# Performance work log

Measured on AMD Instinct MI355X. Metric: run time of the kernel, lower is better.

Reference implementation:

```python
import jax, jax.numpy as jnp
import numpy as np

TOP_K = 2


def setup_inputs() -> dict:
    key = jax.random.key(0)
    ks = jax.random.split(key, 5)
    B, S, D, F, E = 2, 2048, 1024, 3584, 8
    scale_in = 1.0 / np.sqrt(D)
    scale_f = 1.0 / np.sqrt(F)
    return {
        "hidden_states": jax.random.normal(ks[0], (B, S, D), dtype=jnp.float32),
        "gate_w": jax.random.normal(ks[1], (E, D), dtype=jnp.float32) * scale_in,
        "w1": jax.random.normal(ks[2], (E, F, D), dtype=jnp.float32) * scale_in,
        "w3": jax.random.normal(ks[3], (E, F, D), dtype=jnp.float32) * scale_in,
        "w2": jax.random.normal(ks[4], (E, D, F), dtype=jnp.float32) * scale_f,
    }


def _routing_weights(logits):
    # softmax over experts, select top-k, renormalize (Mixtral semantics)
    probs = jax.nn.softmax(logits, axis=-1)          # [T, E]
    topv, topi = jax.lax.top_k(probs, TOP_K)          # [T, k]
    topv = topv / jnp.sum(topv, axis=-1, keepdims=True)
    T, E = logits.shape
    w = jnp.zeros((T, E), dtype=logits.dtype)
    w = w.at[jnp.arange(T)[:, None], topi].set(topv)  # dense [T, E] routing weights
    return w


def reference(hidden_states, gate_w, w1, w3, w2):
    B, S, D = hidden_states.shape
    x = hidden_states.reshape(-1, D)                  # [T, D]
    logits = x @ gate_w.T                             # [T, E]
    rw = _routing_weights(logits)                     # [T, E]
    E = gate_w.shape[0]
    out = jnp.zeros_like(x)
    for e in range(E):                                # fixed small expert count
        h = jax.nn.silu(x @ w1[e].T) * (x @ w3[e].T)  # [T, F]
        out = out + rw[:, e:e + 1] * (h @ w2[e].T)    # [T, D]
    return out.reshape(B, S, D)
```

## Files before the change

### kernel.cpp

```cpp
#include <hip/hip_runtime.h>
#include <hip/hip_bf16.h>


#define T_TOK 4096
#define DIM   1024
#define FF    3584
#define NE    8
#define CAP   (T_TOK*2 + NE*256)

#define OFF_TOPI   256UL
#define OFF_TOPW   33024UL
#define OFF_ROWTOK 65792UL
#define OFF_TOKPOS 106752UL
#define OFF_W1B    147712UL
#define OFF_W3B    (OFF_W1B + 58720256UL)
#define OFF_W2B    OFF_W1B
#define OFF_RES    OFF_W3B
#define OFF_H      (OFF_W1B + 117440512UL)
#define WS_NEED    (OFF_H + 73400320UL)

using f32x4 = __attribute__((ext_vector_type(4))) float;
using s16x8 = __attribute__((ext_vector_type(8))) short;

__device__ __forceinline__ ushort f2b(float f) {
    __hip_bfloat16 b = __float2bfloat16(f);
    ushort u; __builtin_memcpy(&u, &b, 2); return u;
}
__device__ __forceinline__ float blo(uint u){ u <<= 16; float f; __builtin_memcpy(&f,&u,4); return f; }
__device__ __forceinline__ float bhi(uint u){ u &= 0xFFFF0000u; float f; __builtin_memcpy(&f,&u,4); return f; }
__device__ __forceinline__ void gl_lds16(const ushort* g, ushort* l) {
    __builtin_amdgcn_global_load_lds(
        (const __attribute__((address_space(1))) void*)g,
        (__attribute__((address_space(3))) void*)l, 16, 0, 0);
}
__device__ __forceinline__ uint4 pack8(float4 v0, float4 v1) {
    uint4 o;
    o.x = f2b(v0.x) | ((uint)f2b(v0.y) << 16);
    o.y = f2b(v0.z) | ((uint)f2b(v0.w) << 16);
    o.z = f2b(v1.x) | ((uint)f2b(v1.y) << 16);
    o.w = f2b(v1.z) | ((uint)f2b(v1.w) << 16);
    return o;
}

#define VMC(n) asm volatile("s_waitcnt vmcnt(" #n ")" ::: "memory")
#define BAR()  __builtin_amdgcn_s_barrier()

__global__ __launch_bounds__(256)
void k_route(const float* __restrict__ x, const float* __restrict__ gw,
             int* __restrict__ topi, float* __restrict__ topw,
             int* __restrict__ counts, ushort* __restrict__ xb)
{
    __shared__ float gws[NE*DIM];
    const int tid = threadIdx.x;
    for (int i = tid; i < NE*DIM/4; i += 256)
        ((float4*)gws)[i] = ((const float4*)gw)[i];
    __syncthreads();

    const int lane = tid & 63, wid = tid >> 6;
    const int t = blockIdx.x*4 + wid;

    float4 xr[4];
    const float4* xrow = (const float4*)(x + (size_t)t*DIM) + lane*4;
    #pragma unroll
    for (int i = 0; i < 4; ++i) xr[i] = xrow[i];

    uint4* xbd = (uint4*)(xb + (size_t)t*DIM);
    xbd[lane*2]   = pack8(xr[0], xr[1]);
    xbd[lane*2+1] = pack8(xr[2], xr[3]);

    float lg[NE];
    #pragma unroll
    for (int e = 0; e < NE; ++e) {
        const float4* g4 = (const float4*)(gws + e*DIM) + lane*4;
        float s = 0.f;
        #pragma unroll
        for (int i = 0; i < 4; ++i) {
            float4 g = g4[i];
            s += xr[i].x*g.x + xr[i].y*g.y + xr[i].z*g.z + xr[i].w*g.w;
        }
        #pragma unroll
        for (int off = 32; off; off >>= 1) s += __shfl_xor(s, off);
        lg[e] = s;
    }
    if (lane == 0) {
        float b1 = -1e30f, b2 = -1e30f; int i1 = 0, i2 = 0;
        #pragma unroll
        for (int e = 0; e < NE; ++e) {
            float v = lg[e];
            if (v > b1)      { b2 = b1; i2 = i1; b1 = v; i1 = e; }
            else if (v > b2) { b2 = v; i2 = e; }
        }
        float p2 = __expf(b2 - b1);
        float inv = 1.f / (1.f + p2);
        topi[2*t]   = i1; topi[2*t+1] = i2;
        topw[2*t]   = inv; topw[2*t+1] = p2*inv;
        atomicAdd(&counts[i1], 1); atomicAdd(&counts[i2], 1);
    }
}

__global__ void k_scan(const int* __restrict__ counts, int* __restrict__ offs,
                       int* __restrict__ rowTok)
{
    if (threadIdx.x == 0) {
        int acc = 0; offs[0] = 0;
        for (int e = 0; e < NE; ++e) {
            int p = (counts[e] + 255) & ~255;
            acc += p; offs[e+1] = acc;
        }
    }
    for (int i = threadIdx.x; i < CAP; i += blockDim.x) rowTok[i] = -1;
}

__global__ __launch_bounds__(256)
void k_scatter(const int* __restrict__ topi,
               const int* __restrict__ offs, int* __restrict__ cursor,
               int* __restrict__ rowTok, int* __restrict__ tokPos)
{
    int t = blockIdx.x*256 + threadIdx.x;
    #pragma unroll
    for (int j = 0; j < 2; ++j) {
        int e = topi[2*t + j];
        int pos = offs[e] + atomicAdd(&cursor[e], 1);
        rowTok[pos] = t;
        tokPos[2*t + j] = pos;
    }
}

__global__ __launch_bounds__(256)
void k_cvt(const float* __restrict__ src, ushort* __restrict__ dst)
{
    size_t i = (size_t)blockIdx.x*256 + threadIdx.x;
    float4 v0 = ((const float4*)src)[2*i], v1 = ((const float4*)src)[2*i+1];
    ((uint4*)dst)[i] = pack8(v0, v1);
}

#define CVT_HALF ((NE*FF*DIM/8)/256)
__global__ __launch_bounds__(256)
void k_cvt2(const float* __restrict__ w1, const float* __restrict__ w3,
            ushort* __restrict__ w1b, ushort* __restrict__ w3b)
{
    int b = blockIdx.x;
    const float* src; ushort* dst;
    if (b < CVT_HALF) { src = w1; dst = w1b; }
    else              { src = w3; dst = w3b; b -= CVT_HALF; }
    size_t i = (size_t)b*256 + threadIdx.x;
    float4 v0 = ((const float4*)src)[2*i], v1 = ((const float4*)src)[2*i+1];
    ((uint4*)dst)[i] = pack8(v0, v1);
}

#define G1_SLOT 12288
__global__ __launch_bounds__(256, 2)
void k_gemm1(const ushort* __restrict__ xb,
             const ushort* __restrict__ w1b, const ushort* __restrict__ w3b,
             const int* __restrict__ offs, const int* __restrict__ rowTok,
             ushort* __restrict__ hout)
{
    __shared__ __align__(16) ushort L[3*G1_SLOT];
    const int sb = blockIdx.x;
    const int rowStart = blockIdx.y * 256;
    if (rowStart >= offs[8]) return;
    int e = 0;
    #pragma unroll
    for (int k = 1; k < NE; ++k) if (rowStart >= offs[k]) e = k;

    const int tid = threadIdx.x, lane = tid & 63, wid = tid >> 6;
    const int wr = wid >> 1, wc = wid & 1;
    const int lo = lane & 15, hi = lane >> 4;

    const int srow = lane >> 2;
    const int sch  = (lane & 3) ^ ((lane >> 3) & 3);
    const ushort* aS[4];
    #pragma unroll
    for (int j = 0; j < 4; ++j) {
        int tk = rowTok[rowStart + j*64 + wid*16 + srow]; if (tk < 0) tk = 0;
        aS[j] = xb + (size_t)tk*DIM + sch*8;
    }
    const ushort* bS[2];
    bS[0] = w1b + ((size_t)e*FF + sb*64 + wid*16 + srow)*DIM + sch*8;
    bS[1] = w3b + ((size_t)e*FF + sb*64 + wid*16 + srow)*DIM + sch*8;
    ushort* const dA = L + wid*512;
    ushort* const dB = L + 8192 + wid*512;

    const int sig = (lo >> 1) & 3;
    const int roff = ((hi ^ sig) * 8);
    int rdA[8], rdB[4];
    #pragma unroll
    for (int m = 0; m < 8; ++m) rdA[m] = (wr*128 + m*16 + lo)*32 + roff;
    #pragma unroll
    for (int n = 0; n < 2; ++n) {
        rdB[n]   = 8192 + (wc*32 + n*16 + lo)*32 + roff;
        rdB[n+2] = 8192 + (64 + wc*32 + n*16 + lo)*32 + roff;
    }

    f32x4 acc[8][4];
    #pragma unroll
    for (int m = 0; m < 8; ++m)
        #pragma unroll
        for (int n = 0; n < 4; ++n) acc[m][n] = (f32x4)(0.f);

    #pragma unroll
    for (int t0 = 0; t0 < 2; ++t0) {
        #pragma unroll
        for (int j = 0; j < 4; ++j) gl_lds16(aS[j] + t0*32, dA + t0*G1_SLOT + j*2048);
        #pragma unroll
        for (int j = 0; j < 2; ++j) gl_lds16(bS[j] + t0*32, dB + t0*G1_SLOT + j*2048);
    }
    VMC(6);
    BAR();

    const int NK = DIM/32;
    int cur = 0, nxt = 2;
    for (int t = 0; t < NK; ++t) {
        const ushort* Lb = L + cur*G1_SLOT;
        const bool pf = (t + 2 < NK);
        s16x8 a[8], b[4];
        #pragma unroll
        for (int n = 0; n < 4; ++n) b[n] = *(const s16x8*)(Lb + rdB[n]);
        #pragma unroll
        for (int m = 0; m < 8; ++m) a[m] = *(const s16x8*)(Lb + rdA[m]);
        if (pf) {
            #pragma unroll
            for (int j = 0; j < 4; ++j)
                gl_lds16(aS[j] + (t+2)*32, dA + nxt*G1_SLOT + j*2048);
            gl_lds16(bS[0] + (t+2)*32, dB + nxt*G1_SLOT);
            gl_lds16(bS[1] + (t+2)*32, dB + nxt*G1_SLOT + 2048);
        }
        BAR();
        __builtin_amdgcn_s_setprio(1);
        #pragma unroll
        for (int m = 0; m < 8; ++m)
            #pragma unroll
            for (int n = 0; n < 4; ++n)
                acc[m][n] = __builtin_amdgcn_mfma_f32_16x16x32_bf16(a[m], b[n], acc[m][n], 0, 0, 0);
        __builtin_amdgcn_s_setprio(0);
        if (t < NK-2) { VMC(6); } else { VMC(0); }
        BAR();
        cur = (cur == 2) ? 0 : cur + 1;
        nxt = (nxt == 2) ? 0 : nxt + 1;
    }

    #pragma unroll
    for (int m = 0; m < 8; ++m)
        #pragma unroll
        for (int p = 0; p < 2; ++p) {
            f32x4 v1 = acc[m][p], v3 = acc[m][p+2];
            int f = sb*64 + wc*32 + p*16 + lo;
            #pragma unroll
            for (int j = 0; j < 4; ++j) {
                int row = rowStart + wr*128 + m*16 + hi*4 + j;
                float s = v1[j];
                float val = (s / (1.f + __expf(-s))) * v3[j];
                hout[(size_t)row*FF + f] = f2b(val);
            }
        }
}

__global__ __launch_bounds__(256, 2)
void k_gemm2(const ushort* __restrict__ h, const ushort* __restrict__ w2b,
             const int* __restrict__ offs, ushort* __restrict__ res)
{
    __shared__ __align__(16) ushort L[3*G1_SLOT];
    const int dc = blockIdx.x * 128;
    const int rowStart = blockIdx.y * 256;
    if (rowStart >= offs[8]) return;
    int e = 0;
    #pragma unroll
    for (int k = 1; k < NE; ++k) if (rowStart >= offs[k]) e = k;
    const int kbase = blockIdx.z * (FF/2);

    const int tid = threadIdx.x, lane = tid & 63, wid = tid >> 6;
    const int wr = wid >> 1, wc = wid & 1;
    const int lo = lane & 15, hi = lane >> 4;

    const int srow = lane >> 2;
    const int sch  = (lane & 3) ^ ((lane >> 3) & 3);
    const ushort* aS[4];
    #pragma unroll
    for (int j = 0; j < 4; ++j)
        aS[j] = h + (size_t)(rowStart + j*64 + wid*16 + srow)*FF + kbase + sch*8;
    const ushort* bS[2];
    #pragma unroll
    for (int j = 0; j < 2; ++j)
        bS[j] = w2b + ((size_t)e*DIM + dc + j*64 + wid*16 + srow)*FF + kbase + sch*8;
    ushort* const dA = L + wid*512;
    ushort* const dB = L + 8192 + wid*512;

    const int sig = (lo >> 1) & 3;
    const int roff = ((hi ^ sig) * 8);
    int rdA[8], rdB[4];
    #pragma unroll
    for (int m = 0; m < 8; ++m) rdA[m] = (wr*128 + m*16 + lo)*32 + roff;
    #pragma unroll
    for (int n = 0; n < 4; ++n) rdB[n] = 8192 + (wc*64 + n*16 + lo)*32 + roff;

    f32x4 acc[8][4];
    #pragma unroll
    for (int m = 0; m < 8; ++m)
        #pragma unroll
        for (int n = 0; n < 4; ++n) acc[m][n] = (f32x4)(0.f);

    #pragma unroll
    for (int t0 = 0; t0 < 2; ++t0) {
        #pragma unroll
        for (int j = 0; j < 4; ++j) gl_lds16(aS[j] + t0*32, dA + t0*G1_SLOT + j*2048);
        #pragma unroll
        for (int j = 0; j < 2; ++j) gl_lds16(bS[j] + t0*32, dB + t0*G1_SLOT + j*2048);
    }
    VMC(6);
    BAR();

    const int NK = (FF/2)/32;
    int cur = 0, nxt = 2;
    for (int t = 0; t < NK; ++t) {
        const ushort* Lb = L + cur*G1_SLOT;
        const bool pf = (t + 2 < NK);
        s16x8 a[8], b[4];
        #pragma unroll
        for (int n = 0; n < 4; ++n) b[n] = *(const s16x8*)(Lb + rdB[n]);
        #pragma unroll
        for (int m = 0; m < 8; ++m) a[m] = *(const s16x8*)(Lb + rdA[m]);
        if (pf) {
            #pragma unroll
            for (int j = 0; j < 4; ++j)
                gl_lds16(aS[j] + (t+2)*32, dA + nxt*G1_SLOT + j*2048);
            gl_lds16(bS[0] + (t+2)*32, dB + nxt*G1_SLOT);
            gl_lds16(bS[1] + (t+2)*32, dB + nxt*G1_SLOT + 2048);
        }
        BAR();
        __builtin_amdgcn_s_setprio(1);
        #pragma unroll
        for (int m = 0; m < 8; ++m)
            #pragma unroll
            for (int n = 0; n < 4; ++n)
                acc[m][n] = __builtin_amdgcn_mfma_f32_16x16x32_bf16(a[m], b[n], acc[m][n], 0, 0, 0);
        __builtin_amdgcn_s_setprio(0);
        if (t < NK-2) { VMC(6); } else { VMC(0); }
        BAR();
        cur = (cur == 2) ? 0 : cur + 1;
        nxt = (nxt == 2) ? 0 : nxt + 1;
    }

    ushort* rz = res + (size_t)blockIdx.z * CAP * DIM;
    #pragma unroll
    for (int m = 0; m < 8; ++m)
        #pragma unroll
        for (int j = 0; j < 4; ++j) {
            int prow = rowStart + wr*128 + m*16 + hi*4 + j;
            #pragma unroll
            for (int n = 0; n < 4; ++n) {
                int d = dc + wc*64 + n*16 + lo;
                rz[(size_t)prow*DIM + d] = f2b(acc[m][n][j]);
            }
        }
}

__global__ __launch_bounds__(256)
void k_combine(const ushort* __restrict__ res, const int* __restrict__ tokPos,
               const float* __restrict__ topw, float* __restrict__ out)
{
    int i = blockIdx.x*256 + threadIdx.x;
    int t = i >> 7;
    int g = i & 127;
    int pA = tokPos[2*t], pB = tokPos[2*t+1];
    float wA = topw[2*t], wB = topw[2*t+1];
    const ushort* res1 = res + (size_t)CAP * DIM;
    uint4 a0 = *(const uint4*)(res  + (size_t)pA*DIM + g*8);
    uint4 a1 = *(const uint4*)(res1 + (size_t)pA*DIM + g*8);
    uint4 b0 = *(const uint4*)(res  + (size_t)pB*DIM + g*8);
    uint4 b1 = *(const uint4*)(res1 + (size_t)pB*DIM + g*8);
    float4 o0, o1;
    o0.x = wA*(blo(a0.x)+blo(a1.x)) + wB*(blo(b0.x)+blo(b1.x));
    o0.y = wA*(bhi(a0.x)+bhi(a1.x)) + wB*(bhi(b0.x)+bhi(b1.x));
    o0.z = wA*(blo(a0.y)+blo(a1.y)) + wB*(blo(b0.y)+blo(b1.y));
    o0.w = wA*(bhi(a0.y)+bhi(a1.y)) + wB*(bhi(b0.y)+bhi(b1.y));
    o1.x = wA*(blo(a0.z)+blo(a1.z)) + wB*(blo(b0.z)+blo(b1.z));
    o1.y = wA*(bhi(a0.z)+bhi(a1.z)) + wB*(bhi(b0.z)+bhi(b1.z));
    o1.z = wA*(blo(a0.w)+blo(a1.w)) + wB*(blo(b0.w)+blo(b1.w));
    o1.w = wA*(bhi(a0.w)+bhi(a1.w)) + wB*(bhi(b0.w)+bhi(b1.w));
    float4* dst = (float4*)(out + (size_t)t*DIM + g*8);
    dst[0] = o0; dst[1] = o1;
}

extern "C" void kernel_launch(void* const* d_in, const int* in_sizes, int n_in,
                              void* d_out, int out_size, void* d_ws, size_t ws_size,
                              hipStream_t stream)
{
    const float* x  = (const float*)d_in[0];
    const float* gw = (const float*)d_in[1];
    const float* w1 = (const float*)d_in[2];
    const float* w3 = (const float*)d_in[3];
    const float* w2 = (const float*)d_in[4];
    float* out = (float*)d_out;
    char* ws = (char*)d_ws;
    if (ws_size < WS_NEED) return;

    int*    counts = (int*)ws;
    int*    cursor = counts + 8;
    int*    offs   = counts + 16;
    int*    topi   = (int*)  (ws + OFF_TOPI);
    float*  topw   = (float*)(ws + OFF_TOPW);
    int*    rowTok = (int*)  (ws + OFF_ROWTOK);
    int*    tokPos = (int*)  (ws + OFF_TOKPOS);
    ushort* w1b    = (ushort*)(ws + OFF_W1B);
    ushort* w3b    = (ushort*)(ws + OFF_W3B);
    ushort* w2b    = (ushort*)(ws + OFF_W2B);
    ushort* res    = (ushort*)(ws + OFF_RES);
    ushort* h      = (ushort*)(ws + OFF_H);
    ushort* xb     = (ushort*)d_out;

    hipMemsetAsync(ws, 0, 256, stream);

    k_route  <<<T_TOK/4, 256, 0, stream>>>(x, gw, topi, topw, counts, xb);
    k_scan   <<<1, 256, 0, stream>>>(counts, offs, rowTok);
    k_scatter<<<T_TOK/256, 256, 0, stream>>>(topi, offs, cursor, rowTok, tokPos);
    k_cvt2   <<<2*CVT_HALF, 256, 0, stream>>>(w1, w3, w1b, w3b);
    k_gemm1  <<<dim3(56, CAP/256), 256, 0, stream>>>(xb, w1b, w3b, offs, rowTok, h);
    k_cvt    <<<(NE*DIM*FF/8)/256, 256, 0, stream>>>(w2, w2b);
    k_gemm2  <<<dim3(8, CAP/256, 2), 256, 0, stream>>>(h, w2b, offs, res);
    k_combine<<<(T_TOK*DIM/8)/256, 256, 0, stream>>>(res, tokPos, topw, out);
}
```

Baseline: 494.1 us.

## Restructure gemm1 to 8-wave blocks with K=64 tiles and interleaved load/MFMA phases

k_gemm1 now launches 512 threads (8 waves, one block per CU) instead of 256, and each wave owns a 64x64 output slice, so per-wave accumulators shrink from 8x4 to 4x4. The K step grows from 32 to 64 with a wider XOR swizzle, and each iteration is split into four barrier-separated phases that interleave LDS fragment reads and global-to-LDS prefetches with MFMA groups. The aim is to cut register pressure, raise waves per CU, and spread memory traffic across the compute. The cost is more barriers per K step and less scheduling freedom for the compiler; gemm2 only has its LDS slot constant renamed.

```diff
diff --git a/kernel.cpp b/kernel.cpp
--- a/kernel.cpp
+++ b/kernel.cpp
@@ -148,14 +148,14 @@
     ((uint4*)dst)[i] = pack8(v0, v1);
 }
 
-#define G1_SLOT 12288
-__global__ __launch_bounds__(256, 2)
+#define G1S 24576
+__global__ __launch_bounds__(512, 1)
 void k_gemm1(const ushort* __restrict__ xb,
              const ushort* __restrict__ w1b, const ushort* __restrict__ w3b,
              const int* __restrict__ offs, const int* __restrict__ rowTok,
              ushort* __restrict__ hout)
 {
-    __shared__ __align__(16) ushort L[3*G1_SLOT];
+    __shared__ __align__(16) ushort L[3*G1S];
     const int sb = blockIdx.x;
     const int rowStart = blockIdx.y * 256;
     if (rowStart >= offs[8]) return;
@@ -163,75 +163,125 @@
     #pragma unroll
     for (int k = 1; k < NE; ++k) if (rowStart >= offs[k]) e = k;
 
-    const int tid = threadIdx.x, lane = tid & 63, wid = tid >> 6;
+    const int tid = threadIdx.x;
+    const int lane = tid & 63, wid = tid >> 6;
     const int wr = wid >> 1, wc = wid & 1;
     const int lo = lane & 15, hi = lane >> 4;
 
-    const int srow = lane >> 2;
-    const int sch  = (lane & 3) ^ ((lane >> 3) & 3);
+    const int srow8 = tid >> 3;
+    const int gch   = (tid & 7) ^ ((tid >> 4) & 7);
     const ushort* aS[4];
     #pragma unroll
     for (int j = 0; j < 4; ++j) {
-        int tk = rowTok[rowStart + j*64 + wid*16 + srow]; if (tk < 0) tk = 0;
-        aS[j] = xb + (size_t)tk*DIM + sch*8;
+        int tk = rowTok[rowStart + j*64 + srow8]; if (tk < 0) tk = 0;
+        aS[j] = xb + (size_t)tk*DIM + gch*8;
     }
     const ushort* bS[2];
-    bS[0] = w1b + ((size_t)e*FF + sb*64 + wid*16 + srow)*DIM + sch*8;
-    bS[1] = w3b + ((size_t)e*FF + sb*64 + wid*16 + srow)*DIM + sch*8;
-    ushort* const dA = L + wid*512;
-    ushort* const dB = L + 8192 + wid*512;
-
-    const int sig = (lo >> 1) & 3;
-    const int roff = ((hi ^ sig) * 8);
-    int rdA[8], rdB[4];
-    #pragma unroll
-    for (int m = 0; m < 8; ++m) rdA[m] = (wr*128 + m*16 + lo)*32 + roff;
+    bS[0] = w1b + ((size_t)e*FF + sb*64 + srow8)*DIM + gch*8;
+    bS[1] = w3b + ((size_t)e*FF + sb*64 + srow8)*DIM + gch*8;
+    const int dAo = wid*512;
+    const int dBo = 16384 + wid*512;
+
+    const int c0 = (hi ^ ((lo >> 1) & 7)) * 8;
+    int rdA[4], rdB[4];
+    #pragma unroll
+    for (int m = 0; m < 4; ++m) rdA[m] = (wr*64 + m*16 + lo)*64 + c0;
     #pragma unroll
     for (int n = 0; n < 2; ++n) {
-        rdB[n]   = 8192 + (wc*32 + n*16 + lo)*32 + roff;
-        rdB[n+2] = 8192 + (64 + wc*32 + n*16 + lo)*32 + roff;
-    }
-
-    f32x4 acc[8][4];
-    #pragma unroll
-    for (int m = 0; m < 8; ++m)
+        rdB[n]   = 16384 + (wc*32 + n*16 + lo)*64 + c0;
+        rdB[n+2] = 16384 + (64 + wc*32 + n*16 + lo)*64 + c0;
+    }
+
+    f32x4 acc[4][4];
+    #pragma unroll
+    for (int m = 0; m < 4; ++m)
         #pragma unroll
         for (int n = 0; n < 4; ++n) acc[m][n] = (f32x4)(0.f);
 
     #pragma unroll
     for (int t0 = 0; t0 < 2; ++t0) {
         #pragma unroll
-        for (int j = 0; j < 4; ++j) gl_lds16(aS[j] + t0*32, dA + t0*G1_SLOT + j*2048);
-        #pragma unroll
-        for (int j = 0; j < 2; ++j) gl_lds16(bS[j] + t0*32, dB + t0*G1_SLOT + j*2048);
+        for (int j = 0; j < 4; ++j) gl_lds16(aS[j] + t0*64, L + t0*G1S + dAo + j*4096);
+        #pragma unroll
+        for (int j = 0; j < 2; ++j) gl_lds16(bS[j] + t0*64, L + t0*G1S + dBo + j*4096);
     }
     VMC(6);
     BAR();
 
-    const int NK = DIM/32;
+    const int NK = DIM/64;
     int cur = 0, nxt = 2;
     for (int t = 0; t < NK; ++t) {
-        const ushort* Lb = L + cur*G1_SLOT;
+        const ushort* Lb = L + cur*G1S;
+        ushort* Ln = L + nxt*G1S;
         const bool pf = (t + 2 < NK);
-        s16x8 a[8], b[4];
-        #pragma unroll
-        for (int n = 0; n < 4; ++n) b[n] = *(const s16x8*)(Lb + rdB[n]);
-        #pragma unroll
-        for (int m = 0; m < 8; ++m) a[m] = *(const s16x8*)(Lb + rdA[m]);
+        const int go = (t + 2)*64;
+        s16x8 a0, a1, b0, b1, b2, b3;
+        b0 = *(const s16x8*)(Lb + rdB[0]); b1 = *(const s16x8*)(Lb + rdB[1]);
+        b2 = *(const s16x8*)(Lb + rdB[2]); b3 = *(const s16x8*)(Lb + rdB[3]);
+        a0 = *(const s16x8*)(Lb + rdA[0]); a1 = *(const s16x8*)(Lb + rdA[1]);
         if (pf) {
-            #pragma unroll
-            for (int j = 0; j < 4; ++j)
-                gl_lds16(aS[j] + (t+2)*32, dA + nxt*G1_SLOT + j*2048);
-            gl_lds16(bS[0] + (t+2)*32, dB + nxt*G1_SLOT);
-            gl_lds16(bS[1] + (t+2)*32, dB + nxt*G1_SLOT + 2048);
+            gl_lds16(aS[0] + go, Ln + dAo);
+            gl_lds16(aS[1] + go, Ln + dAo + 4096);
         }
         BAR();
         __builtin_amdgcn_s_setprio(1);
-        #pragma unroll
-        for (int m = 0; m < 8; ++m)
-            #pragma unroll
-            for (int n = 0; n < 4; ++n)
-                acc[m][n] = __builtin_amdgcn_mfma_f32_16x16x32_bf16(a[m], b[n], acc[m][n], 0, 0, 0);
+        acc[0][0] = __builtin_amdgcn_mfma_f32_16x16x32_bf16(a0, b0, acc[0][0], 0, 0, 0);
+        acc[0][1] = __builtin_amdgcn_mfma_f32_16x16x32_bf16(a0, b1, acc[0][1], 0, 0, 0);
+        acc[0][2] = __builtin_amdgcn_mfma_f32_16x16x32_bf16(a0, b2, acc[0][2], 0, 0, 0);
+        acc[0][3] = __builtin_amdgcn_mfma_f32_16x16x32_bf16(a0, b3, acc[0][3], 0, 0, 0);
+        acc[1][0] = __builtin_amdgcn_mfma_f32_16x16x32_bf16(a1, b0, acc[1][0], 0, 0, 0);
+        acc[1][1] = __builtin_amdgcn_mfma_f32_16x16x32_bf16(a1, b1, acc[1][1], 0, 0, 0);
+        acc[1][2] = __builtin_amdgcn_mfma_f32_16x16x32_bf16(a1, b2, acc[1][2], 0, 0, 0);
+        acc[1][3] = __builtin_amdgcn_mfma_f32_16x16x32_bf16(a1, b3, acc[1][3], 0, 0, 0);
+        __builtin_amdgcn_s_setprio(0);
+        BAR();
+        a0 = *(const s16x8*)(Lb + rdA[2]); a1 = *(const s16x8*)(Lb + rdA[3]);
+        if (pf) {
+            gl_lds16(aS[2] + go, Ln + dAo + 2*4096);
+            gl_lds16(aS[3] + go, Ln + dAo + 3*4096);
+        }
+        BAR();
+        __builtin_amdgcn_s_setprio(1);
+        acc[2][0] = __builtin_amdgcn_mfma_f32_16x16x32_bf16(a0, b0, acc[2][0], 0, 0, 0);
+        acc[2][1] = __builtin_amdgcn_mfma_f32_16x16x32_bf16(a0, b1, acc[2][1], 0, 0, 0);
+        acc[2][2] = __builtin_amdgcn_mfma_f32_16x16x32_bf16(a0, b2, acc[2][2], 0, 0, 0);
+        acc[2][3] = __builtin_amdgcn_mfma_f32_16x16x32_bf16(a0, b3, acc[2][3], 0, 0, 0);
+        acc[3][0] = __builtin_amdgcn_mfma_f32_16x16x32_bf16(a1, b0, acc[3][0], 0, 0, 0);
+        acc[3][1] = __builtin_amdgcn_mfma_f32_16x16x32_bf16(a1, b1, acc[3][1], 0, 0, 0);
+        acc[3][2] = __builtin_amdgcn_mfma_f32_16x16x32_bf16(a1, b2, acc[3][2], 0, 0, 0);
+        acc[3][3] = __builtin_amdgcn_mfma_f32_16x16x32_bf16(a1, b3, acc[3][3], 0, 0, 0);
+        __builtin_amdgcn_s_setprio(0);
+        BAR();
+        b0 = *(const s16x8*)(Lb + (rdB[0]^32)); b1 = *(const s16x8*)(Lb + (rdB[1]^32));
+        b2 = *(const s16x8*)(Lb + (rdB[2]^32)); b3 = *(const s16x8*)(Lb + (rdB[3]^32));
+        a0 = *(const s16x8*)(Lb + (rdA[0]^32)); a1 = *(const s16x8*)(Lb + (rdA[1]^32));
+        if (pf) {
+            gl_lds16(bS[0] + go, Ln + dBo);
+            gl_lds16(bS[1] + go, Ln + dBo + 4096);
+        }
+        BAR();
+        __builtin_amdgcn_s_setprio(1);
+        acc[0][0] = __builtin_amdgcn_mfma_f32_16x16x32_bf16(a0, b0, acc[0][0], 0, 0, 0);
+        acc[0][1] = __builtin_amdgcn_mfma_f32_16x16x32_bf16(a0, b1, acc[0][1], 0, 0, 0);
+        acc[0][2] = __builtin_amdgcn_mfma_f32_16x16x32_bf16(a0, b2, acc[0][2], 0, 0, 0);
+        acc[0][3] = __builtin_amdgcn_mfma_f32_16x16x32_bf16(a0, b3, acc[0][3], 0, 0, 0);
+        acc[1][0] = __builtin_amdgcn_mfma_f32_16x16x32_bf16(a1, b0, acc[1][0], 0, 0, 0);
+        acc[1][1] = __builtin_amdgcn_mfma_f32_16x16x32_bf16(a1, b1, acc[1][1], 0, 0, 0);
+        acc[1][2] = __builtin_amdgcn_mfma_f32_16x16x32_bf16(a1, b2, acc[1][2], 0, 0, 0);
+        acc[1][3] = __builtin_amdgcn_mfma_f32_16x16x32_bf16(a1, b3, acc[1][3], 0, 0, 0);
+        __builtin_amdgcn_s_setprio(0);
+        BAR();
+        a0 = *(const s16x8*)(Lb + (rdA[2]^32)); a1 = *(const s16x8*)(Lb + (rdA[3]^32));
+        BAR();
+        __builtin_amdgcn_s_setprio(1);
+        acc[2][0] = __builtin_amdgcn_mfma_f32_16x16x32_bf16(a0, b0, acc[2][0], 0, 0, 0);
+        acc[2][1] = __builtin_amdgcn_mfma_f32_16x16x32_bf16(a0, b1, acc[2][1], 0, 0, 0);
+        acc[2][2] = __builtin_amdgcn_mfma_f32_16x16x32_bf16(a0, b2, acc[2][2], 0, 0, 0);
+        acc[2][3] = __builtin_amdgcn_mfma_f32_16x16x32_bf16(a0, b3, acc[2][3], 0, 0, 0);
+        acc[3][0] = __builtin_amdgcn_mfma_f32_16x16x32_bf16(a1, b0, acc[3][0], 0, 0, 0);
+        acc[3][1] = __builtin_amdgcn_mfma_f32_16x16x32_bf16(a1, b1, acc[3][1], 0, 0, 0);
+        acc[3][2] = __builtin_amdgcn_mfma_f32_16x16x32_bf16(a1, b2, acc[3][2], 0, 0, 0);
+        acc[3][3] = __builtin_amdgcn_mfma_f32_16x16x32_bf16(a1, b3, acc[3][3], 0, 0, 0);
         __builtin_amdgcn_s_setprio(0);
         if (t < NK-2) { VMC(6); } else { VMC(0); }
         BAR();
@@ -240,14 +290,14 @@
     }
 
     #pragma unroll
-    for (int m = 0; m < 8; ++m)
+    for (int m = 0; m < 4; ++m)
         #pragma unroll
         for (int p = 0; p < 2; ++p) {
             f32x4 v1 = acc[m][p], v3 = acc[m][p+2];
             int f = sb*64 + wc*32 + p*16 + lo;
             #pragma unroll
             for (int j = 0; j < 4; ++j) {
-                int row = rowStart + wr*128 + m*16 + hi*4 + j;
+                int row = rowStart + wr*64 + m*16 + hi*4 + j;
                 float s = v1[j];
                 float val = (s / (1.f + __expf(-s))) * v3[j];
                 hout[(size_t)row*FF + f] = f2b(val);
@@ -255,11 +305,12 @@
         }
 }
 
+#define G2_SLOT 12288
 __global__ __launch_bounds__(256, 2)
 void k_gemm2(const ushort* __restrict__ h, const ushort* __restrict__ w2b,
              const int* __restrict__ offs, ushort* __restrict__ res)
 {
-    __shared__ __align__(16) ushort L[3*G1_SLOT];
+    __shared__ __align__(16) ushort L[3*G2_SLOT];
     const int dc = blockIdx.x * 128;
     const int rowStart = blockIdx.y * 256;
     if (rowStart >= offs[8]) return;
@@ -302,9 +353,9 @@
     #pragma unroll
     for (int t0 = 0; t0 < 2; ++t0) {
         #pragma unroll
-        for (int j = 0; j < 4; ++j) gl_lds16(aS[j] + t0*32, dA + t0*G1_SLOT + j*2048);
-        #pragma unroll
-        for (int j = 0; j < 2; ++j) gl_lds16(bS[j] + t0*32, dB + t0*G1_SLOT + j*2048);
+        for (int j = 0; j < 4; ++j) gl_lds16(aS[j] + t0*32, dA + t0*G2_SLOT + j*2048);
+        #pragma unroll
+        for (int j = 0; j < 2; ++j) gl_lds16(bS[j] + t0*32, dB + t0*G2_SLOT + j*2048);
     }
     VMC(6);
     BAR();
@@ -312,7 +363,7 @@
     const int NK = (FF/2)/32;
     int cur = 0, nxt = 2;
     for (int t = 0; t < NK; ++t) {
-        const ushort* Lb = L + cur*G1_SLOT;
+        const ushort* Lb = L + cur*G2_SLOT;
         const bool pf = (t + 2 < NK);
         s16x8 a[8], b[4];
         #pragma unroll
@@ -322,9 +373,9 @@
         if (pf) {
             #pragma unroll
             for (int j = 0; j < 4; ++j)
-                gl_lds16(aS[j] + (t+2)*32, dA + nxt*G1_SLOT + j*2048);
-            gl_lds16(bS[0] + (t+2)*32, dB + nxt*G1_SLOT);
-            gl_lds16(bS[1] + (t+2)*32, dB + nxt*G1_SLOT + 2048);
+                gl_lds16(aS[j] + (t+2)*32, dA + nxt*G2_SLOT + j*2048);
+            gl_lds16(bS[0] + (t+2)*32, dB + nxt*G2_SLOT);
+            gl_lds16(bS[1] + (t+2)*32, dB + nxt*G2_SLOT + 2048);
         }
         BAR();
         __builtin_amdgcn_s_setprio(1);
@@ -414,7 +465,7 @@
     k_scan   <<<1, 256, 0, stream>>>(counts, offs, rowTok);
     k_scatter<<<T_TOK/256, 256, 0, stream>>>(topi, offs, cursor, rowTok, tokPos);
     k_cvt2   <<<2*CVT_HALF, 256, 0, stream>>>(w1, w3, w1b, w3b);
-    k_gemm1  <<<dim3(56, CAP/256), 256, 0, stream>>>(xb, w1b, w3b, offs, rowTok, h);
+    k_gemm1  <<<dim3(56, CAP/256), 512, 0, stream>>>(xb, w1b, w3b, offs, rowTok, h);
     k_cvt    <<<(NE*DIM*FF/8)/256, 256, 0, stream>>>(w2, w2b);
     k_gemm2  <<<dim3(8, CAP/256, 2), 256, 0, stream>>>(h, w2b, offs, res);
     k_combine<<<(T_TOK*DIM/8)/256, 256, 0, stream>>>(res, tokPos, topw, out);
```

Measured after the change: 515.4 us. 4.3% more time.
